# Kernel tuning notes

Measured on AMD Instinct MI355X. Metric: run time of the kernel, lower is better.

The kernel has to match this reference:

```python
import jax, jax.numpy as jnp
import numpy as np

N = 100000          # nodes
E = 1600000         # edges (before self-loops)
F_IN = 128          # raw node features
TOPO = 8            # topological feature dim
HEADS1, HID1 = 8, 8 # conv1: 8 heads x 8 channels, concat -> 64
C_OUT = 40          # classes (conv2: 1 head, no concat)
NEG_SLOPE = 0.2     # PyG GATConv leaky_relu slope


def setup_inputs() -> dict:
    key = jax.random.key(0)
    ks = jax.random.split(key, 12)
    x = jax.random.normal(ks[0], (N, F_IN), jnp.float32)
    topo = jax.random.normal(ks[1], (N, TOPO), jnp.float32)
    edge_index = jax.random.randint(ks[2], (2, E), 0, N, jnp.int32)
    s = 0.1
    W1 = jax.random.normal(ks[3], (F_IN + TOPO, HEADS1 * HID1), jnp.float32) * s
    a_src1 = jax.random.normal(ks[4], (HEADS1, HID1), jnp.float32) * s
    a_dst1 = jax.random.normal(ks[5], (HEADS1, HID1), jnp.float32) * s
    b1 = jnp.zeros((HEADS1 * HID1,), jnp.float32)
    W2 = jax.random.normal(ks[6], (HEADS1 * HID1, C_OUT), jnp.float32) * s
    a_src2 = jax.random.normal(ks[7], (1, C_OUT), jnp.float32) * s
    a_dst2 = jax.random.normal(ks[8], (1, C_OUT), jnp.float32) * s
    b2 = jnp.zeros((C_OUT,), jnp.float32)
    return {"x": x, "topo": topo, "edge_index": edge_index,
            "W1": W1, "a_src1": a_src1, "a_dst1": a_dst1, "b1": b1,
            "W2": W2, "a_src2": a_src2, "a_dst2": a_dst2, "b2": b2}


def _gat_conv(x, src, dst, W, a_src, a_dst, b, heads, concat):
    # x: [N, Fin]; src/dst: [Etot] (self-loops already included)
    n = x.shape[0]
    h = (x @ W).reshape(n, heads, -1)                 # [N, H, C]
    alpha_s = jnp.sum(h * a_src[None], axis=-1)       # [N, H]
    alpha_d = jnp.sum(h * a_dst[None], axis=-1)       # [N, H]
    e = jax.nn.leaky_relu(alpha_s[src] + alpha_d[dst], NEG_SLOPE)  # [Etot, H]
    # segment softmax over destination nodes (numerically stable)
    m = jax.ops.segment_max(e, dst, num_segments=n)   # [N, H]
    ex = jnp.exp(e - m[dst])
    z = jax.ops.segment_sum(ex, dst, num_segments=n)  # [N, H]
    alpha = ex / (z[dst] + 1e-16)                     # [Etot, H]
    out = jax.ops.segment_sum(h[src] * alpha[..., None], dst, num_segments=n)  # [N,H,C]
    out = out.reshape(n, -1) if concat else out.mean(axis=1)
    return out + b


def reference(x, topo, edge_index, W1, a_src1, a_dst1, b1, W2, a_src2, a_dst2, b2):
    n = x.shape[0]
    loops = jnp.arange(n, dtype=edge_index.dtype)
    src = jnp.concatenate([edge_index[0], loops])  # PyG add_self_loops=True
    dst = jnp.concatenate([edge_index[1], loops])
    h = jnp.concatenate([x, topo], axis=1)         # [N, F_IN + TOPO]
    # dropout is identity in eval mode
    h = jax.nn.elu(_gat_conv(h, src, dst, W1, a_src1, a_dst1, b1, HEADS1, True))
    logits = _gat_conv(h, src, dst, W2, a_src2, a_dst2, b2, 1, False)
    return jax.nn.log_softmax(logits, axis=1)
```

## Files before the change

kernel.cpp:

```cpp
#include <hip/hip_runtime.h>
#include <math.h>


#define NBUK_MAX 512
#define BIN_CHUNK 4096
#define BUK_CAP 4608

typedef unsigned short ushort_t;

__device__ inline unsigned int f2bf(float f) {
    unsigned int u = __float_as_uint(f);
    u += 0x7FFFu + ((u >> 16) & 1u);
    return u >> 16;
}
__device__ inline float bf_lo(unsigned int u) {
    return __uint_as_float(u << 16);
}
__device__ inline float bf_hi(unsigned int u) {
    return __uint_as_float(u & 0xFFFF0000u);
}
__device__ inline float lrelu_exp(float q) {
    return __expf(q >= 0.f ? q : 0.2f * q);
}

__device__ inline int wave_incl_scan(int v, int lane) {
    #pragma unroll
    for (int ofs = 1; ofs < 64; ofs <<= 1) {
        int t = __shfl_up(v, ofs);
        if (lane >= ofs) v += t;
    }
    return v;
}

__global__ __launch_bounds__(256) void k_bin(const int* __restrict__ src,
                                             const int* __restrict__ dst,
                                             int* __restrict__ gCursor,
                                             unsigned int* __restrict__ tmp,
                                             int E, int NBUK) {
    __shared__ int lcnt[NBUK_MAX];
    __shared__ int lcur[NBUK_MAX];
    int tid = threadIdx.x;
    int base = blockIdx.x * BIN_CHUNK;
    for (int i = tid; i < NBUK; i += 256) lcnt[i] = 0;
    __syncthreads();
    int d[16];
    #pragma unroll
    for (int q = 0; q < 4; q++) {
        int e = base + q * 1024 + 4 * tid;
        if (e + 3 < E) {
            int4 v = *(const int4*)&dst[e];
            d[4 * q + 0] = v.x; d[4 * q + 1] = v.y;
            d[4 * q + 2] = v.z; d[4 * q + 3] = v.w;
        } else {
            #pragma unroll
            for (int k = 0; k < 4; k++)
                d[4 * q + k] = (e + k < E) ? dst[e + k] : -1;
        }
    }
    #pragma unroll
    for (int k = 0; k < 16; k++)
        if (d[k] >= 0) atomicAdd(&lcnt[d[k] >> 8], 1);
    __syncthreads();
    for (int b = tid; b < NBUK; b += 256) {
        int c = lcnt[b];
        lcur[b] = c ? b * BUK_CAP + atomicAdd(&gCursor[b], c) : 0;
    }
    __syncthreads();
    #pragma unroll
    for (int q = 0; q < 4; q++) {
        int e = base + q * 1024 + 4 * tid;
        int s[4];
        if (e + 3 < E) {
            int4 v = *(const int4*)&src[e];
            s[0] = v.x; s[1] = v.y; s[2] = v.z; s[3] = v.w;
        } else {
            #pragma unroll
            for (int k = 0; k < 4; k++)
                s[k] = (e + k < E) ? src[e + k] : 0;
        }
        #pragma unroll
        for (int k = 0; k < 4; k++) {
            int dd = d[4 * q + k];
            if (dd >= 0) {
                int p = atomicAdd(&lcur[dd >> 8], 1);
                tmp[p] = ((unsigned int)s[k] << 8) | (unsigned int)(dd & 255);
            }
        }
    }
}

__global__ __launch_bounds__(512) void k_fill2(const unsigned int* __restrict__ tmp,
                                               const int* __restrict__ gCursor,
                                               int* __restrict__ rowptr,
                                               int* __restrict__ rowEnd,
                                               int* __restrict__ csr, int N) {
    __shared__ int cnt[256];
    __shared__ int cur[256];
    __shared__ int wsum[4];
    int b = blockIdx.x, tid = threadIdx.x;
    int e0 = b * BUK_CAP;
    int cnt_e = gCursor[b];
    int e1 = e0 + cnt_e;
    if (tid < 256) cnt[tid] = 0;
    __syncthreads();
    {
        int nq = cnt_e >> 2;
        const uint4* t4 = (const uint4*)(tmp + e0);
        for (int q = tid; q < nq; q += 512) {
            uint4 v = t4[q];
            atomicAdd(&cnt[v.x & 255u], 1);
            atomicAdd(&cnt[v.y & 255u], 1);
            atomicAdd(&cnt[v.z & 255u], 1);
            atomicAdd(&cnt[v.w & 255u], 1);
        }
        for (int i = (nq << 2) + tid; i < cnt_e; i += 512)
            atomicAdd(&cnt[tmp[e0 + i] & 255u], 1);
    }
    __syncthreads();
    if (tid < 256) {
        int lane = tid & 63, wv = tid >> 6;
        int v = cnt[tid];
        int incl = wave_incl_scan(v, lane);
        if (lane == 63) wsum[wv] = incl;
        cnt[tid] = incl - v;
    }
    __syncthreads();
    if (tid < 256) {
        int wv = tid >> 6;
        int woff = 0;
        for (int i = 0; i < wv; i++) woff += wsum[i];
        int excl = woff + cnt[tid];
        int node = b * 256 + tid;
        int start = e0 + excl;
        cur[tid] = start;
        if (node < N) {
            rowptr[node] = start;
        }
    }
    __syncthreads();
    if (tid < 256) {
        int node = b * 256 + tid;
        if (node < N) rowEnd[node] = (tid < 255) ? cur[tid + 1] : e1;
    }
    __syncthreads();
    for (int i = e0 + tid; i < e1; i += 512) {
        unsigned int t = tmp[i];
        int p = atomicAdd(&cur[t & 255u], 1);
        csr[p] = (int)(t >> 8);
    }
}

__global__ __launch_bounds__(256) void k_xform1(const float* __restrict__ x,
                                                const float* __restrict__ topo,
                                                const float* __restrict__ W1,
                                                const float* __restrict__ asrc,
                                                const float* __restrict__ adst,
                                                ushort_t* __restrict__ h1b,
                                                float* __restrict__ as1,
                                                float* __restrict__ ad1, int N) {
    __shared__ float XT[136 * 64];
    __shared__ float WS[136 * 64];
    int tid = threadIdx.x;
    int n0 = blockIdx.x * 64;
    {
        const float4* W4 = (const float4*)W1;
        float4* WS4 = (float4*)WS;
        for (int i = tid; i < 2176; i += 256) WS4[i] = W4[i];
    }
    {
        const float4* x4 = (const float4*)x;
        for (int i = tid; i < 2048; i += 256) {
            int node = i & 63, k4 = i >> 6;
            int gn = n0 + node; if (gn > N - 1) gn = N - 1;
            float4 v = x4[(size_t)gn * 32 + k4];
            int k = k4 * 4;
            XT[(k + 0) * 64 + node] = v.x;
            XT[(k + 1) * 64 + node] = v.y;
            XT[(k + 2) * 64 + node] = v.z;
            XT[(k + 3) * 64 + node] = v.w;
        }
        const float4* t4 = (const float4*)topo;
        if (tid < 128) {
            int node = tid & 63, j4 = tid >> 6;
            int gn = n0 + node; if (gn > N - 1) gn = N - 1;
            float4 v = t4[(size_t)gn * 2 + j4];
            int k = 128 + j4 * 4;
            XT[(k + 0) * 64 + node] = v.x;
            XT[(k + 1) * 64 + node] = v.y;
            XT[(k + 2) * 64 + node] = v.z;
            XT[(k + 3) * 64 + node] = v.w;
        }
    }
    __syncthreads();
    int ci = tid & 15, ni = tid >> 4;
    int nb = ni * 4, cb = ci * 4;
    float acc[16];
    #pragma unroll
    for (int i = 0; i < 16; i++) acc[i] = 0.f;
    #pragma unroll 4
    for (int k = 0; k < 136; k++) {
        float4 xv = *(const float4*)&XT[k * 64 + nb];
        float4 wv = *(const float4*)&WS[k * 64 + cb];
        acc[0]  = fmaf(xv.x, wv.x, acc[0]);  acc[1]  = fmaf(xv.x, wv.y, acc[1]);
        acc[2]  = fmaf(xv.x, wv.z, acc[2]);  acc[3]  = fmaf(xv.x, wv.w, acc[3]);
        acc[4]  = fmaf(xv.y, wv.x, acc[4]);  acc[5]  = fmaf(xv.y, wv.y, acc[5]);
        acc[6]  = fmaf(xv.y, wv.z, acc[6]);  acc[7]  = fmaf(xv.y, wv.w, acc[7]);
        acc[8]  = fmaf(xv.z, wv.x, acc[8]);  acc[9]  = fmaf(xv.z, wv.y, acc[9]);
        acc[10] = fmaf(xv.z, wv.z, acc[10]); acc[11] = fmaf(xv.z, wv.w, acc[11]);
        acc[12] = fmaf(xv.w, wv.x, acc[12]); acc[13] = fmaf(xv.w, wv.y, acc[13]);
        acc[14] = fmaf(xv.w, wv.z, acc[14]); acc[15] = fmaf(xv.w, wv.w, acc[15]);
    }
    int head = cb >> 3;
    #pragma unroll
    for (int i = 0; i < 4; i++) {
        int n = n0 + nb + i;
        unsigned int p0 = f2bf(acc[i * 4 + 0]) | (f2bf(acc[i * 4 + 1]) << 16);
        unsigned int p1 = f2bf(acc[i * 4 + 2]) | (f2bf(acc[i * 4 + 3]) << 16);
        if (n < N) *(uint2*)&h1b[(size_t)n * 64 + cb] = make_uint2(p0, p1);
        float s = 0.f, d = 0.f;
        #pragma unroll
        for (int j = 0; j < 4; j++) {
            s = fmaf(acc[i * 4 + j], asrc[cb + j], s);
            d = fmaf(acc[i * 4 + j], adst[cb + j], d);
        }
        s += __shfl_xor(s, 1);
        d += __shfl_xor(d, 1);
        if ((ci & 1) == 0 && n < N) {
            as1[n * 8 + head] = s;
            ad1[n * 8 + head] = d;
        }
    }
}

#define AGG_FMA(W_, U_)                                           \
    {                                                             \
        acc[0] = fmaf(W_, bf_lo(U_.x), acc[0]);                   \
        acc[1] = fmaf(W_, bf_hi(U_.x), acc[1]);                   \
        acc[2] = fmaf(W_, bf_lo(U_.y), acc[2]);                   \
        acc[3] = fmaf(W_, bf_hi(U_.y), acc[3]);                   \
        acc[4] = fmaf(W_, bf_lo(U_.z), acc[4]);                   \
        acc[5] = fmaf(W_, bf_hi(U_.z), acc[5]);                   \
        acc[6] = fmaf(W_, bf_lo(U_.w), acc[6]);                   \
        acc[7] = fmaf(W_, bf_hi(U_.w), acc[7]);                   \
        z += W_;                                                  \
    }

#define AGG1_GATHER(EIDX, SE_, AV_, UU_)                                     \
    int SE_ = __shfl(cv, nbase + ((EIDX) < d ? (EIDX) : dm1));               \
    SE_ = d > 0 ? SE_ : 0;                                                   \
    float AV_ = as1[SE_ * 8 + head];                                         \
    uint4 UU_ = *(const uint4*)(h1c + (((unsigned)SE_ << 7) + hoff));

#define AGG1_COMP(EIDX, AV_, UU_)                                            \
    {                                                                        \
        float w_ = (EIDX) < d ? lrelu_exp(AV_ + adv) : 0.f;                  \
        AGG_FMA(w_, UU_);                                                    \
    }

__global__ __launch_bounds__(256) void k_agg1(const ushort_t* __restrict__ h1b,
                                              const float* __restrict__ as1,
                                              const float* __restrict__ ad1,
                                              const float* __restrict__ b1,
                                              const int* __restrict__ rowptr,
                                              const int* __restrict__ rowEnd,
                                              const int* __restrict__ csr,
                                              float* __restrict__ h2, int N) {
    int tid = threadIdx.x, lane = tid & 63;
    int nbase0 = blockIdx.x * 8 + ((tid >> 6) << 1);
    if (nbase0 >= N) return;
    int nid = lane >> 5;
    int nbase = nid << 5;
    int l32 = lane & 31;
    int g = (lane >> 3) & 3;
    int head = lane & 7;
    int n = nbase0 + nid;
    bool valid = n < N;
    int nc = valid ? n : N - 1;
    const char* h1c = (const char*)h1b;
    unsigned hoff = (unsigned)head << 4;
    float adv = ad1[nc * 8 + head];
    float acc[8];
    #pragma unroll
    for (int k = 0; k < 8; k++) acc[k] = 0.f;
    float z = 0.f;

    int j0 = rowptr[nc], j1 = rowEnd[nc];
    int d = valid ? (j1 - j0) : 0;
    int dm1 = d > 0 ? d - 1 : 0;
    int dx = __shfl_xor(d, 32);
    int dmax = d > dx ? d : dx;
    int cv = csr[j0 + (l32 < d ? l32 : dm1)];

    {
        float w = lrelu_exp(as1[nc * 8 + head] + adv);
        if (g == 0 && valid) {
            uint4 u = *(const uint4*)(h1c + (((unsigned)nc << 7) + hoff));
            acc[0] = w * bf_lo(u.x); acc[1] = w * bf_hi(u.x);
            acc[2] = w * bf_lo(u.y); acc[3] = w * bf_hi(u.y);
            acc[4] = w * bf_lo(u.z); acc[5] = w * bf_hi(u.z);
            acc[6] = w * bf_lo(u.w); acc[7] = w * bf_hi(u.w);
            z = w;
        }
    }
    if (dmax > 0) {
        int e0 = g, e1 = 4 + g, e2 = 8 + g, e3 = 12 + g, e4 = 16 + g, e5 = 20 + g;
        AGG1_GATHER(e0, s0, a0, u0)
        AGG1_GATHER(e1, s1, a1, u1)
        AGG1_GATHER(e2, s2, a2, u2)
        AGG1_GATHER(e3, s3, a3, u3)
        AGG1_GATHER(e4, s4, a4, u4)
        AGG1_GATHER(e5, s5, a5, u5)
        AGG1_COMP(e0, a0, u0)
        if (dmax > 4)  AGG1_COMP(e1, a1, u1)
        if (dmax > 8)  AGG1_COMP(e2, a2, u2)
        if (dmax > 12) AGG1_COMP(e3, a3, u3)
        if (dmax > 16) AGG1_COMP(e4, a4, u4)
        if (dmax > 20) AGG1_COMP(e5, a5, u5)
        if (dmax > 24) {
            int e6 = 24 + g, e7 = 28 + g;
            AGG1_GATHER(e6, s6, a6, u6)
            AGG1_GATHER(e7, s7, a7, u7)
            AGG1_COMP(e6, a6, u6)
            if (dmax > 28) AGG1_COMP(e7, a7, u7)
            if (dmax > 32) {
                for (int eb = 32; eb < dmax; eb += 4) {
                    int e = eb + g;
                    int idx = e < d ? e : dm1;
                    int se = csr[j0 + idx];
                    se = d > 0 ? se : 0;
                    float av = as1[se * 8 + head];
                    uint4 u = *(const uint4*)(h1c + (((unsigned)se << 7) + hoff));
                    float w = e < d ? lrelu_exp(av + adv) : 0.f;
                    AGG_FMA(w, u);
                }
            }
        }
    }
    #pragma unroll
    for (int k = 0; k < 8; k++) {
        acc[k] += __shfl_xor(acc[k], 8);
        acc[k] += __shfl_xor(acc[k], 16);
    }
    z += __shfl_xor(z, 8); z += __shfl_xor(z, 16);
    if (g == 0 && valid) {
        float inv = 1.f / (z + 1e-16f);
        float o[8];
        #pragma unroll
        for (int k = 0; k < 8; k++) {
            float v = acc[k] * inv + b1[head * 8 + k];
            o[k] = v > 0.f ? v : (__expf(v) - 1.f);
        }
        float4* dp = (float4*)&h2[(size_t)n * 64 + head * 8];
        dp[0] = make_float4(o[0], o[1], o[2], o[3]);
        dp[1] = make_float4(o[4], o[5], o[6], o[7]);
    }
}

__global__ __launch_bounds__(256) void k_xform2(const float* __restrict__ h2,
                                                const float* __restrict__ W2,
                                                const float* __restrict__ asrc2,
                                                const float* __restrict__ adst2,
                                                ushort_t* __restrict__ gb,
                                                float* __restrict__ as2,
                                                float* __restrict__ ad2, int N) {
    __shared__ float XT[64 * 64];
    __shared__ float WS[64 * 40];
    int tid = threadIdx.x;
    int n0 = blockIdx.x * 64;
    {
        const float4* W4 = (const float4*)W2;
        float4* WS4 = (float4*)WS;
        for (int i = tid; i < 640; i += 256) WS4[i] = W4[i];
    }
    {
        const float4* h4 = (const float4*)h2;
        for (int i = tid; i < 1024; i += 256) {
            int node = i & 63, k4 = i >> 6;
            int gn = n0 + node; if (gn > N - 1) gn = N - 1;
            float4 v = h4[(size_t)gn * 16 + k4];
            int k = k4 * 4;
            XT[(k + 0) * 64 + node] = v.x;
            XT[(k + 1) * 64 + node] = v.y;
            XT[(k + 2) * 64 + node] = v.z;
            XT[(k + 3) * 64 + node] = v.w;
        }
    }
    __syncthreads();
    int ci = tid & 15, ni = tid >> 4;
    int nb = ni * 4, cb = ci * 4;
    float acc[16];
    #pragma unroll
    for (int i = 0; i < 16; i++) acc[i] = 0.f;
    if (ci < 10) {
        #pragma unroll 4
        for (int k = 0; k < 64; k++) {
            float4 xv = *(const float4*)&XT[k * 64 + nb];
            float4 wv = *(const float4*)&WS[k * 40 + cb];
            acc[0]  = fmaf(xv.x, wv.x, acc[0]);  acc[1]  = fmaf(xv.x, wv.y, acc[1]);
            acc[2]  = fmaf(xv.x, wv.z, acc[2]);  acc[3]  = fmaf(xv.x, wv.w, acc[3]);
            acc[4]  = fmaf(xv.y, wv.x, acc[4]);  acc[5]  = fmaf(xv.y, wv.y, acc[5]);
            acc[6]  = fmaf(xv.y, wv.z, acc[6]);  acc[7]  = fmaf(xv.y, wv.w, acc[7]);
            acc[8]  = fmaf(xv.z, wv.x, acc[8]);  acc[9]  = fmaf(xv.z, wv.y, acc[9]);
            acc[10] = fmaf(xv.z, wv.z, acc[10]); acc[11] = fmaf(xv.z, wv.w, acc[11]);
            acc[12] = fmaf(xv.w, wv.x, acc[12]); acc[13] = fmaf(xv.w, wv.y, acc[13]);
            acc[14] = fmaf(xv.w, wv.z, acc[14]); acc[15] = fmaf(xv.w, wv.w, acc[15]);
        }
    }
    #pragma unroll
    for (int i = 0; i < 4; i++) {
        int n = n0 + nb + i;
        if (ci < 10 && n < N) {
            unsigned int p0 = f2bf(acc[i * 4 + 0]) | (f2bf(acc[i * 4 + 1]) << 16);
            unsigned int p1 = f2bf(acc[i * 4 + 2]) | (f2bf(acc[i * 4 + 3]) << 16);
            *(uint2*)&gb[(size_t)n * 40 + cb] = make_uint2(p0, p1);
        }
        float s = 0.f, d = 0.f;
        if (ci < 10) {
            #pragma unroll
            for (int j = 0; j < 4; j++) {
                s = fmaf(acc[i * 4 + j], asrc2[cb + j], s);
                d = fmaf(acc[i * 4 + j], adst2[cb + j], d);
            }
        }
        s += __shfl_xor(s, 1); s += __shfl_xor(s, 2);
        s += __shfl_xor(s, 4); s += __shfl_xor(s, 8);
        d += __shfl_xor(d, 1); d += __shfl_xor(d, 2);
        d += __shfl_xor(d, 4); d += __shfl_xor(d, 8);
        if (ci == 0 && n < N) { as2[n] = s; ad2[n] = d; }
    }
}

#define AGG2_C2(B_)                                                            \
    {                                                                          \
        int ew0 = (B_) * 12 + lm12, ew1 = ew0 + 12;                            \
        int sw0 = __shfl(cv, ew0 < d ? ew0 : dm1);                             \
        int sw1 = __shfl(cv, ew1 < d ? ew1 : dm1);                             \
        float av0 = as2[sw0];                                                  \
        float av1 = as2[sw1];                                                  \
        int e00 = (B_) * 12 + gi0, e01 = (B_) * 12 + gi1;                      \
        int e02 = (B_) * 12 + gi2, e03 = (B_) * 12 + gi3;                      \
        int s00 = __shfl(cv, e00 < d ? e00 : dm1);                             \
        int s01 = __shfl(cv, e01 < d ? e01 : dm1);                             \
        int s02 = __shfl(cv, e02 < d ? e02 : dm1);                             \
        int s03 = __shfl(cv, e03 < d ? e03 : dm1);                             \
        int s10 = __shfl(cv, e00 + 12 < d ? e00 + 12 : dm1);                   \
        int s11 = __shfl(cv, e01 + 12 < d ? e01 + 12 : dm1);                   \
        int s12 = __shfl(cv, e02 + 12 < d ? e02 + 12 : dm1);                   \
        int s13 = __shfl(cv, e03 + 12 < d ? e03 + 12 : dm1);                   \
        unsigned int u00 = *(const unsigned int*)(gbc + ((unsigned)s00 * 80u + coff)); \
        unsigned int u01 = *(const unsigned int*)(gbc + ((unsigned)s01 * 80u + coff)); \
        unsigned int u02 = *(const unsigned int*)(gbc + ((unsigned)s02 * 80u + coff)); \
        unsigned int u03 = *(const unsigned int*)(gbc + ((unsigned)s03 * 80u + coff)); \
        unsigned int u10 = *(const unsigned int*)(gbc + ((unsigned)s10 * 80u + coff)); \
        unsigned int u11 = *(const unsigned int*)(gbc + ((unsigned)s11 * 80u + coff)); \
        unsigned int u12 = *(const unsigned int*)(gbc + ((unsigned)s12 * 80u + coff)); \
        unsigned int u13 = *(const unsigned int*)(gbc + ((unsigned)s13 * 80u + coff)); \
        float wall0 = (ew0 < d) ? lrelu_exp(av0 + add) : 0.f;                  \
        float wall1 = (ew1 < d) ? lrelu_exp(av1 + add) : 0.f;                  \
        float w00 = __shfl(wall0, gi0), w01 = __shfl(wall0, gi1);              \
        float w02 = __shfl(wall0, gi2), w03 = __shfl(wall0, gi3);              \
        float w10 = __shfl(wall1, gi0), w11 = __shfl(wall1, gi1);              \
        float w12 = __shfl(wall1, gi2), w13 = __shfl(wall1, gi3);              \
        acc0 = fmaf(w00, bf_lo(u00), acc0); acc1 = fmaf(w00, bf_hi(u00), acc1); zl += w00; \
        acc0 = fmaf(w01, bf_lo(u01), acc0); acc1 = fmaf(w01, bf_hi(u01), acc1); zl += w01; \
        acc0 = fmaf(w02, bf_lo(u02), acc0); acc1 = fmaf(w02, bf_hi(u02), acc1); zl += w02; \
        acc0 = fmaf(w03, bf_lo(u03), acc0); acc1 = fmaf(w03, bf_hi(u03), acc1); zl += w03; \
        acc0 = fmaf(w10, bf_lo(u10), acc0); acc1 = fmaf(w10, bf_hi(u10), acc1); zl += w10; \
        acc0 = fmaf(w11, bf_lo(u11), acc0); acc1 = fmaf(w11, bf_hi(u11), acc1); zl += w11; \
        acc0 = fmaf(w12, bf_lo(u12), acc0); acc1 = fmaf(w12, bf_hi(u12), acc1); zl += w12; \
        acc0 = fmaf(w13, bf_lo(u13), acc0); acc1 = fmaf(w13, bf_hi(u13), acc1); zl += w13; \
    }

__global__ __launch_bounds__(256) void k_agg2(const ushort_t* __restrict__ gb,
                                              const float* __restrict__ as2,
                                              const float* __restrict__ ad2,
                                              const float* __restrict__ b2,
                                              const int* __restrict__ rowptr,
                                              const int* __restrict__ rowEnd,
                                              const int* __restrict__ csr,
                                              float* __restrict__ out, int N) {
    int tid = threadIdx.x, lane = tid & 63;
    int n = blockIdx.x * 4 + (tid >> 6);
    if (n >= N) return;
    int g = lane / 20, p = lane % 20;
    int c0 = 2 * p;
    const char* gbc = (const char*)gb;
    unsigned coff = (unsigned)(p << 2);
    int lm12 = lane % 12;
    int gi0 = (0 + g) < 12 ? (0 + g) : 11;
    int gi1 = (3 + g) < 12 ? (3 + g) : 11;
    int gi2 = (6 + g) < 12 ? (6 + g) : 11;
    int gi3 = (9 + g) < 12 ? (9 + g) : 11;
    float add = ad2[n];
    float acc0 = 0.f, acc1 = 0.f, zl = 0.f;

    int j0 = rowptr[n], j1 = rowEnd[n];
    int d = j1 - j0;
    int dm1 = d > 0 ? d - 1 : 0;
    int cv = (d > 0) ? csr[j0 + (lane < d ? lane : dm1)] : 0;

    {
        float e0 = as2[n] + add;
        float w = lrelu_exp(e0);
        if (g == 0) {
            unsigned int u = *(const unsigned int*)(gbc + ((unsigned)n * 80u + coff));
            acc0 = w * bf_lo(u); acc1 = w * bf_hi(u); zl = w;
        }
    }
    if (d > 0) {
        AGG2_C2(0);
        if (d > 24) {
            AGG2_C2(2);
            if (d > 48) {
                for (int j = j0 + 48; j < j1; j += 12) {
                    int m = j1 - j;
                    int idx = lm12 < m ? lm12 : m - 1;
                    int cvt = csr[j + idx];
                    float av = as2[cvt];
                    float wall = (lm12 < m) ? lrelu_exp(av + add) : 0.f;
                    #pragma unroll
                    for (int i = 0; i < 4; i++) {
                        int e = 3 * i + g;
                        int gi = e < 12 ? e : 11;
                        int gim = gi < m ? gi : m - 1;
                        int s = __shfl(cvt, gim);
                        unsigned int u = *(const unsigned int*)(gbc + ((unsigned)s * 80u + coff));
                        float w = __shfl(wall, gi);
                        acc0 = fmaf(w, bf_lo(u), acc0);
                        acc1 = fmaf(w, bf_hi(u), acc1);
                        zl += w;
                    }
                }
            }
        }
    }
    float A0 = acc0 + __shfl(acc0, (lane + 20) & 63) + __shfl(acc0, (lane + 40) & 63);
    float A1 = acc1 + __shfl(acc1, (lane + 20) & 63) + __shfl(acc1, (lane + 40) & 63);
    float Z  = zl + __shfl(zl, (lane + 20) & 63) + __shfl(zl, (lane + 40) & 63);
    float l0 = 0.f, l1 = 0.f;
    bool active = (lane < 20);
    if (active) {
        float inv = 1.f / (Z + 1e-16f);
        l0 = A0 * inv + b2[c0];
        l1 = A1 * inv + b2[c0 + 1];
    }
    float mv = active ? fmaxf(l0, l1) : -INFINITY;
    #pragma unroll
    for (int ofs = 1; ofs < 32; ofs <<= 1) mv = fmaxf(mv, __shfl_xor(mv, ofs));
    float ev = active ? (__expf(l0 - mv) + __expf(l1 - mv)) : 0.f;
    #pragma unroll
    for (int ofs = 1; ofs < 32; ofs <<= 1) ev += __shfl_xor(ev, ofs);
    if (active) {
        float ls = mv + __logf(ev);
        *(float2*)&out[(size_t)n * 40 + c0] = make_float2(l0 - ls, l1 - ls);
    }
}

extern "C" void kernel_launch(void* const* d_in, const int* in_sizes, int n_in,
                              void* d_out, int out_size, void* d_ws, size_t ws_size,
                              hipStream_t stream) {
    const float* x    = (const float*)d_in[0];
    const float* topo = (const float*)d_in[1];
    const int*   ei   = (const int*)d_in[2];
    const float* W1   = (const float*)d_in[3];
    const float* a_s1 = (const float*)d_in[4];
    const float* a_d1 = (const float*)d_in[5];
    const float* b1   = (const float*)d_in[6];
    const float* W2   = (const float*)d_in[7];
    const float* a_s2 = (const float*)d_in[8];
    const float* a_d2 = (const float*)d_in[9];
    const float* b2   = (const float*)d_in[10];
    float* out = (float*)d_out;

    int N = in_sizes[0] / 128;
    int E = in_sizes[2] / 2;
    const int* esrc = ei;
    const int* edst = ei + E;
    int NBUK = (N + 255) / 256;
    size_t cap = (size_t)NBUK * BUK_CAP;

    char* ws = (char*)d_ws;
    size_t off = 0;
    auto alloc = [&](size_t bytes) -> void* {
        void* p = ws + off;
        off = (off + bytes + 255) & ~(size_t)255;
        return p;
    };
    ushort_t* h1b  = (ushort_t*)alloc((size_t)N * 64 * 2);
    float* as1     = (float*)alloc((size_t)N * 8 * 4);
    float* ad1     = (float*)alloc((size_t)N * 8 * 4);
    float* h2      = (float*)alloc((size_t)N * 64 * 4);
    ushort_t* gb   = (ushort_t*)alloc((size_t)N * 40 * 2);
    float* as2     = (float*)alloc((size_t)N * 4);
    float* ad2     = (float*)alloc((size_t)N * 4);
    int*   rowptr  = (int*)alloc((size_t)N * 4);
    int*   rowEnd  = (int*)alloc((size_t)N * 4);
    int*   csr     = (int*)alloc(cap * 4);
    unsigned int* tmp = (unsigned int*)alloc(cap * 4);
    int* gCursor   = (int*)alloc((size_t)NBUK * 4);

    hipMemsetAsync(gCursor, 0, (size_t)NBUK * 4, stream);
    int nbin = (E + BIN_CHUNK - 1) / BIN_CHUNK;
    k_bin<<<nbin, 256, 0, stream>>>(esrc, edst, gCursor, tmp, E, NBUK);
    k_fill2<<<NBUK, 512, 0, stream>>>(tmp, gCursor, rowptr, rowEnd, csr, N);

    int nbg = (N + 63) / 64;
    int nb8 = (N + 7) / 8;
    int nb4 = (N + 3) / 4;
    k_xform1<<<nbg, 256, 0, stream>>>(x, topo, W1, a_s1, a_d1, h1b, as1, ad1, N);
    k_agg1<<<nb8, 256, 0, stream>>>(h1b, as1, ad1, b1, rowptr, rowEnd, csr, h2, N);
    k_xform2<<<nbg, 256, 0, stream>>>(h2, W2, a_s2, a_d2, gb, as2, ad2, N);
    k_agg2<<<nb4, 256, 0, stream>>>(gb, as2, ad2, b2, rowptr, rowEnd, csr, out, N);
}
```

Before: 289.1 us.

## Process two nodes per wavefront in layer-2 aggregation with 8-byte gathers

Measured after the change: 281.0 us. 1.03x faster.

```diff
diff --git a/kernel.cpp b/kernel.cpp
--- a/kernel.cpp
+++ b/kernel.cpp
@@ -430,45 +430,21 @@
     }
 }
 
-#define AGG2_C2(B_)                                                            \
-    {                                                                          \
-        int ew0 = (B_) * 12 + lm12, ew1 = ew0 + 12;                            \
-        int sw0 = __shfl(cv, ew0 < d ? ew0 : dm1);                             \
-        int sw1 = __shfl(cv, ew1 < d ? ew1 : dm1);                             \
-        float av0 = as2[sw0];                                                  \
-        float av1 = as2[sw1];                                                  \
-        int e00 = (B_) * 12 + gi0, e01 = (B_) * 12 + gi1;                      \
-        int e02 = (B_) * 12 + gi2, e03 = (B_) * 12 + gi3;                      \
-        int s00 = __shfl(cv, e00 < d ? e00 : dm1);                             \
-        int s01 = __shfl(cv, e01 < d ? e01 : dm1);                             \
-        int s02 = __shfl(cv, e02 < d ? e02 : dm1);                             \
-        int s03 = __shfl(cv, e03 < d ? e03 : dm1);                             \
-        int s10 = __shfl(cv, e00 + 12 < d ? e00 + 12 : dm1);                   \
-        int s11 = __shfl(cv, e01 + 12 < d ? e01 + 12 : dm1);                   \
-        int s12 = __shfl(cv, e02 + 12 < d ? e02 + 12 : dm1);                   \
-        int s13 = __shfl(cv, e03 + 12 < d ? e03 + 12 : dm1);                   \
-        unsigned int u00 = *(const unsigned int*)(gbc + ((unsigned)s00 * 80u + coff)); \
-        unsigned int u01 = *(const unsigned int*)(gbc + ((unsigned)s01 * 80u + coff)); \
-        unsigned int u02 = *(const unsigned int*)(gbc + ((unsigned)s02 * 80u + coff)); \
-        unsigned int u03 = *(const unsigned int*)(gbc + ((unsigned)s03 * 80u + coff)); \
-        unsigned int u10 = *(const unsigned int*)(gbc + ((unsigned)s10 * 80u + coff)); \
-        unsigned int u11 = *(const unsigned int*)(gbc + ((unsigned)s11 * 80u + coff)); \
-        unsigned int u12 = *(const unsigned int*)(gbc + ((unsigned)s12 * 80u + coff)); \
-        unsigned int u13 = *(const unsigned int*)(gbc + ((unsigned)s13 * 80u + coff)); \
-        float wall0 = (ew0 < d) ? lrelu_exp(av0 + add) : 0.f;                  \
-        float wall1 = (ew1 < d) ? lrelu_exp(av1 + add) : 0.f;                  \
-        float w00 = __shfl(wall0, gi0), w01 = __shfl(wall0, gi1);              \
-        float w02 = __shfl(wall0, gi2), w03 = __shfl(wall0, gi3);              \
-        float w10 = __shfl(wall1, gi0), w11 = __shfl(wall1, gi1);              \
-        float w12 = __shfl(wall1, gi2), w13 = __shfl(wall1, gi3);              \
-        acc0 = fmaf(w00, bf_lo(u00), acc0); acc1 = fmaf(w00, bf_hi(u00), acc1); zl += w00; \
-        acc0 = fmaf(w01, bf_lo(u01), acc0); acc1 = fmaf(w01, bf_hi(u01), acc1); zl += w01; \
-        acc0 = fmaf(w02, bf_lo(u02), acc0); acc1 = fmaf(w02, bf_hi(u02), acc1); zl += w02; \
-        acc0 = fmaf(w03, bf_lo(u03), acc0); acc1 = fmaf(w03, bf_hi(u03), acc1); zl += w03; \
-        acc0 = fmaf(w10, bf_lo(u10), acc0); acc1 = fmaf(w10, bf_hi(u10), acc1); zl += w10; \
-        acc0 = fmaf(w11, bf_lo(u11), acc0); acc1 = fmaf(w11, bf_hi(u11), acc1); zl += w11; \
-        acc0 = fmaf(w12, bf_lo(u12), acc0); acc1 = fmaf(w12, bf_hi(u12), acc1); zl += w12; \
-        acc0 = fmaf(w13, bf_lo(u13), acc0); acc1 = fmaf(w13, bf_hi(u13), acc1); zl += w13; \
+#define AGG2_G(C_, SE_, AV_, UU_)                                            \
+    int ee##C_ = 3 * (C_) + gg;                                              \
+    int SE_ = __shfl(cv, nbase + (ee##C_ < d ? ee##C_ : dm1));               \
+    SE_ = d > 0 ? SE_ : 0;                                                   \
+    float AV_ = as2[SE_];                                                    \
+    uint2 UU_ = *(const uint2*)(gbc + (unsigned)SE_ * 80u + poff);
+
+#define AGG2_K(C_, AV_, UU_)                                                 \
+    {                                                                        \
+        float w_ = (ee##C_ < d) ? lrelu_exp(AV_ + add) : 0.f;                \
+        acc[0] = fmaf(w_, bf_lo(UU_.x), acc[0]);                             \
+        acc[1] = fmaf(w_, bf_hi(UU_.x), acc[1]);                             \
+        acc[2] = fmaf(w_, bf_lo(UU_.y), acc[2]);                             \
+        acc[3] = fmaf(w_, bf_hi(UU_.y), acc[3]);                             \
+        z += w_;                                                             \
     }
 
 __global__ __launch_bounds__(256) void k_agg2(const ushort_t* __restrict__ gb,
@@ -480,79 +456,118 @@
                                               const int* __restrict__ csr,
                                               float* __restrict__ out, int N) {
     int tid = threadIdx.x, lane = tid & 63;
-    int n = blockIdx.x * 4 + (tid >> 6);
-    if (n >= N) return;
-    int g = lane / 20, p = lane % 20;
-    int c0 = 2 * p;
+    int nbase0 = blockIdx.x * 8 + ((tid >> 6) << 1);
+    if (nbase0 >= N) return;
+    int nid = lane >> 5;
+    int nbase = nid << 5;
+    int l32 = lane & 31;
+    int gg = l32 / 10;
+    int p = l32 - gg * 10;
+    if (gg > 2) { gg = 2; p = 9; }
+    int n = nbase0 + nid;
+    bool valid = n < N;
+    int nc = valid ? n : N - 1;
     const char* gbc = (const char*)gb;
-    unsigned coff = (unsigned)(p << 2);
-    int lm12 = lane % 12;
-    int gi0 = (0 + g) < 12 ? (0 + g) : 11;
-    int gi1 = (3 + g) < 12 ? (3 + g) : 11;
-    int gi2 = (6 + g) < 12 ? (6 + g) : 11;
-    int gi3 = (9 + g) < 12 ? (9 + g) : 11;
-    float add = ad2[n];
-    float acc0 = 0.f, acc1 = 0.f, zl = 0.f;
-
-    int j0 = rowptr[n], j1 = rowEnd[n];
-    int d = j1 - j0;
+    unsigned poff = (unsigned)p << 3;
+    float add = ad2[nc];
+    float acc[4] = {0.f, 0.f, 0.f, 0.f};
+    float z = 0.f;
+
+    int j0 = rowptr[nc], j1 = rowEnd[nc];
+    int d = valid ? (j1 - j0) : 0;
     int dm1 = d > 0 ? d - 1 : 0;
-    int cv = (d > 0) ? csr[j0 + (lane < d ? lane : dm1)] : 0;
-
-    {
-        float e0 = as2[n] + add;
-        float w = lrelu_exp(e0);
-        if (g == 0) {
-            unsigned int u = *(const unsigned int*)(gbc + ((unsigned)n * 80u + coff));
-            acc0 = w * bf_lo(u); acc1 = w * bf_hi(u); zl = w;
-        }
-    }
-    if (d > 0) {
-        AGG2_C2(0);
-        if (d > 24) {
-            AGG2_C2(2);
-            if (d > 48) {
-                for (int j = j0 + 48; j < j1; j += 12) {
-                    int m = j1 - j;
-                    int idx = lm12 < m ? lm12 : m - 1;
-                    int cvt = csr[j + idx];
-                    float av = as2[cvt];
-                    float wall = (lm12 < m) ? lrelu_exp(av + add) : 0.f;
-                    #pragma unroll
-                    for (int i = 0; i < 4; i++) {
-                        int e = 3 * i + g;
-                        int gi = e < 12 ? e : 11;
-                        int gim = gi < m ? gi : m - 1;
-                        int s = __shfl(cvt, gim);
-                        unsigned int u = *(const unsigned int*)(gbc + ((unsigned)s * 80u + coff));
-                        float w = __shfl(wall, gi);
-                        acc0 = fmaf(w, bf_lo(u), acc0);
-                        acc1 = fmaf(w, bf_hi(u), acc1);
-                        zl += w;
-                    }
+    int dxx = __shfl_xor(d, 32);
+    int dmax = d > dxx ? d : dxx;
+    int cv = csr[j0 + (l32 < d ? l32 : dm1)];
+
+    {
+        float w = lrelu_exp(as2[nc] + add);
+        if (gg == 0 && valid) {
+            uint2 u = *(const uint2*)(gbc + (unsigned)nc * 80u + poff);
+            acc[0] = w * bf_lo(u.x); acc[1] = w * bf_hi(u.x);
+            acc[2] = w * bf_lo(u.y); acc[3] = w * bf_hi(u.y);
+            z = w;
+        }
+    }
+    if (dmax > 0) {
+        AGG2_G(0, s0, a0, u0)
+        AGG2_G(1, s1, a1, u1)
+        AGG2_G(2, s2, a2, u2)
+        AGG2_G(3, s3, a3, u3)
+        AGG2_G(4, s4, a4, u4)
+        AGG2_G(5, s5, a5, u5)
+        AGG2_G(6, s6, a6, u6)
+        AGG2_G(7, s7, a7, u7)
+        AGG2_K(0, a0, u0)
+        if (dmax > 3)  AGG2_K(1, a1, u1)
+        if (dmax > 6)  AGG2_K(2, a2, u2)
+        if (dmax > 9)  AGG2_K(3, a3, u3)
+        if (dmax > 12) AGG2_K(4, a4, u4)
+        if (dmax > 15) AGG2_K(5, a5, u5)
+        if (dmax > 18) AGG2_K(6, a6, u6)
+        if (dmax > 21) AGG2_K(7, a7, u7)
+        if (dmax > 24) {
+            AGG2_G(8, s8, a8, u8)
+            AGG2_G(9, s9, a9, u9)
+            AGG2_K(8, a8, u8)
+            if (dmax > 27) AGG2_K(9, a9, u9)
+            if (dmax > 30) {
+                for (int eb = 30; eb < dmax; eb += 3) {
+                    int e = eb + gg;
+                    int idx = e < d ? e : dm1;
+                    int se = csr[j0 + idx];
+                    se = d > 0 ? se : 0;
+                    float av = as2[se];
+                    uint2 u = *(const uint2*)(gbc + (unsigned)se * 80u + poff);
+                    float w = (e < d) ? lrelu_exp(av + add) : 0.f;
+                    acc[0] = fmaf(w, bf_lo(u.x), acc[0]);
+                    acc[1] = fmaf(w, bf_hi(u.x), acc[1]);
+                    acc[2] = fmaf(w, bf_lo(u.y), acc[2]);
+                    acc[3] = fmaf(w, bf_hi(u.y), acc[3]);
+                    z += w;
                 }
             }
         }
     }
-    float A0 = acc0 + __shfl(acc0, (lane + 20) & 63) + __shfl(acc0, (lane + 40) & 63);
-    float A1 = acc1 + __shfl(acc1, (lane + 20) & 63) + __shfl(acc1, (lane + 40) & 63);
-    float Z  = zl + __shfl(zl, (lane + 20) & 63) + __shfl(zl, (lane + 40) & 63);
-    float l0 = 0.f, l1 = 0.f;
-    bool active = (lane < 20);
-    if (active) {
-        float inv = 1.f / (Z + 1e-16f);
-        l0 = A0 * inv + b2[c0];
-        l1 = A1 * inv + b2[c0 + 1];
-    }
-    float mv = active ? fmaxf(l0, l1) : -INFINITY;
-    #pragma unroll
-    for (int ofs = 1; ofs < 32; ofs <<= 1) mv = fmaxf(mv, __shfl_xor(mv, ofs));
-    float ev = active ? (__expf(l0 - mv) + __expf(l1 - mv)) : 0.f;
-    #pragma unroll
-    for (int ofs = 1; ofs < 32; ofs <<= 1) ev += __shfl_xor(ev, ofs);
-    if (active) {
+    #pragma unroll
+    for (int k = 0; k < 4; k++) {
+        float t1 = __shfl(acc[k], lane + 10);
+        float t2 = __shfl(acc[k], lane + 20);
+        acc[k] += t1 + t2;
+    }
+    {
+        float t1 = __shfl(z, lane + 10);
+        float t2 = __shfl(z, lane + 20);
+        z += t1 + t2;
+    }
+    bool act = (l32 < 10) && valid;
+    float l[4];
+    float mv = -INFINITY;
+    if (act) {
+        float inv = 1.f / (z + 1e-16f);
+        #pragma unroll
+        for (int k = 0; k < 4; k++) {
+            l[k] = acc[k] * inv + b2[p * 4 + k];
+            mv = fmaxf(mv, l[k]);
+        }
+    }
+    mv = fmaxf(mv, __shfl_xor(mv, 1));
+    mv = fmaxf(mv, __shfl_xor(mv, 2));
+    mv = fmaxf(mv, __shfl_xor(mv, 4));
+    mv = fmaxf(mv, __shfl_xor(mv, 8));
+    float ev = 0.f;
+    if (act) {
+        #pragma unroll
+        for (int k = 0; k < 4; k++) ev += __expf(l[k] - mv);
+    }
+    ev += __shfl_xor(ev, 1);
+    ev += __shfl_xor(ev, 2);
+    ev += __shfl_xor(ev, 4);
+    ev += __shfl_xor(ev, 8);
+    if (act) {
         float ls = mv + __logf(ev);
-        *(float2*)&out[(size_t)n * 40 + c0] = make_float2(l0 - ls, l1 - ls);
+        float4* dp = (float4*)&out[(size_t)n * 40 + p * 4];
+        dp[0] = make_float4(l[0] - ls, l[1] - ls, l[2] - ls, l[3] - ls);
     }
 }
 
@@ -606,9 +621,8 @@
 
     int nbg = (N + 63) / 64;
     int nb8 = (N + 7) / 8;
-    int nb4 = (N + 3) / 4;
     k_xform1<<<nbg, 256, 0, stream>>>(x, topo, W1, a_s1, a_d1, h1b, as1, ad1, N);
     k_agg1<<<nb8, 256, 0, stream>>>(h1b, as1, ad1, b1, rowptr, rowEnd, csr, h2, N);
     k_xform2<<<nbg, 256, 0, stream>>>(h2, W2, a_s2, a_d2, gb, as2, ad2, N);
-    k_agg2<<<nb4, 256, 0, stream>>>(gb, as2, ad2, b2, rowptr, rowEnd, csr, out, N);
-}
+    k_agg2<<<nb8, 256, 0, stream>>>(gb, as2, ad2, b2, rowptr, rowEnd, csr, out, N);
+}
```
